# Kernel optimization log

Measured on AMD Instinct MI355X. Metric: run time of the kernel, lower is better.

The kernel has to match this reference:

```python
import jax, jax.numpy as jnp
import numpy as np

GCN_DIM = 512
POS_EMB_DIM = 64
K = 8
L = 128  # uttr_len
B = 16
PAIR_FEAT = 2 * GCN_DIM + POS_EMB_DIM


def _pair_indices(L, K):
    # Static (trace-time) construction of the windowed pair list, matching the
    # torch masked_select over the full L*L pair grid: row p = i*L + j keeps
    # pairs with |j - i| <= K, in the same row-major order.
    i = np.repeat(np.arange(L), L)
    j = np.tile(np.arange(L), L)
    rel = j - i
    mask = np.abs(rel) <= K
    return i[mask], j[mask], rel[mask]


def setup_inputs() -> dict:
    key = jax.random.key(0)
    k1, k2, k3, k4, k5, k6, k7 = jax.random.split(key, 7)
    h_emo = jax.random.normal(k1, (B, L, GCN_DIM), dtype=jnp.float32)
    h_cause = jax.random.normal(k2, (B, L, GCN_DIM), dtype=jnp.float32)
    # xavier_uniform for embedding table
    lim_e = np.sqrt(6.0 / (2 * K + 1 + POS_EMB_DIM))
    pos_emb = jax.random.uniform(k3, (2 * K + 1, POS_EMB_DIM), minval=-lim_e, maxval=lim_e, dtype=jnp.float32)
    lim1 = np.sqrt(1.0 / PAIR_FEAT)
    W1 = jax.random.uniform(k4, (PAIR_FEAT, PAIR_FEAT), minval=-lim1, maxval=lim1, dtype=jnp.float32)
    b1 = jax.random.uniform(k5, (PAIR_FEAT,), minval=-lim1, maxval=lim1, dtype=jnp.float32)
    W2 = jax.random.uniform(k6, (1, PAIR_FEAT), minval=-lim1, maxval=lim1, dtype=jnp.float32)
    b2 = jax.random.uniform(k7, (1,), minval=-lim1, maxval=lim1, dtype=jnp.float32)
    return {
        "uttr_output_h_emotion": h_emo,
        "uttr_output_h_cause": h_cause,
        "pos_emb": pos_emb,
        "W1": W1,
        "b1": b1,
        "W2": W2,
        "b2": b2,
    }


def reference(uttr_output_h_emotion, uttr_output_h_cause, pos_emb, W1, b1, W2, b2):
    emo_idx, cau_idx, rel_np = _pair_indices(L, K)  # static numpy, length n
    emo_idx_j = jnp.asarray(emo_idx)
    cau_idx_j = jnp.asarray(cau_idx)
    rel = jnp.asarray(rel_np)  # [n], values in [-K, K]

    # windowed pair gather: couples_h = [H_emo[i] ; H_cause[j]]  -> [B, n, 2*g]
    P = jnp.concatenate(
        [uttr_output_h_emotion[:, emo_idx_j, :], uttr_output_h_cause[:, cau_idx_j, :]],
        axis=2,
    )

    # relative-position embedding + Gaussian kernel smoothing (batch-invariant)
    rel_emb = pos_emb[rel + K]  # [n, pos_emb_dim]
    rel_f = rel.astype(jnp.float32)
    kernel = jnp.exp(-jnp.square(rel_f[:, None] - rel_f[None, :]))  # [n, n]
    smoothed = kernel @ rel_emb  # [n, pos_emb_dim]

    couples = jnp.concatenate(
        [P, jnp.broadcast_to(smoothed[None], (P.shape[0],) + smoothed.shape)], axis=2
    )  # [B, n, PAIR_FEAT]

    h = jax.nn.relu(jnp.einsum("bnf,gf->bng", couples, W1) + b1)
    pred = (jnp.einsum("bnf,of->bno", h, W2) + b2).squeeze(-1)  # [B, n]

    emo_cau_pos = jnp.stack([emo_idx_j + 1, cau_idx_j + 1], axis=1)  # [n, 2], int
    return pred, emo_cau_pos
```

## Files before the change

### kernel.cpp

```cpp
#include <hip/hip_runtime.h>

typedef unsigned short u16;
typedef unsigned int u32;
typedef __attribute__((ext_vector_type(4))) float f32x4;
typedef __attribute__((ext_vector_type(8))) __bf16 bf16x8;
typedef __attribute__((ext_vector_type(4))) u16 u16x4;
typedef __attribute__((ext_vector_type(4))) float f32x4v;

#define LSEQ 128
#define KW 8
#define NP 2104
#define BATCH 16
#define MTOT 33664
#define FDIM 1088
#define GPAD 1152

#define WS_W1P  0ul
#define WS_EMOB 2506752ul
#define WS_CAUB 4603904ul
#define WS_SB   6701056ul
#define WS_TOFF 6738048ul
#define WS_EC   6738560ul

__device__ __forceinline__ u16 f2bf(float x) {
  union { float f; u32 u; } v; v.f = x;
  u32 r = v.u + 0x7fffu + ((v.u >> 16) & 1u);
  return (u16)(r >> 16);
}

__device__ __forceinline__ float bf2f(u16 x) {
  union { u32 u; float f; } v; v.u = ((u32)x) << 16; return v.f;
}

__device__ __forceinline__ void load_lds16(const void* g, void* l) {
  __builtin_amdgcn_global_load_lds(
      (const __attribute__((address_space(1))) void*)g,
      (__attribute__((address_space(3))) void*)l, 16, 0, 0);
}

__global__ __launch_bounds__(256)
void setup_all(const float* __restrict__ emo, const float* __restrict__ cau,
               const float* __restrict__ pos_emb, const float* __restrict__ W1,
               const float* __restrict__ b1,
               u16* __restrict__ W1p, u16* __restrict__ emoB,
               u16* __restrict__ cauB, u16* __restrict__ Sb,
               int* __restrict__ tab_off, float* __restrict__ out_pos) {
  __shared__ float smL[17 * 64];
  const int bx = blockIdx.x;
  const int t = threadIdx.x;
  if (bx < 1224) {
    int idx = bx * 256 + t;
    if (idx >= 313344) return;
    int g = idx / 272;
    int f = (idx - g * 272) * 4;
    u16x4 o;
    if (g < 1088) {
      f32x4v v = *(const f32x4v*)&W1[g * 1088 + f];
      o.x = f2bf(v.x); o.y = f2bf(v.y); o.z = f2bf(v.z); o.w = f2bf(v.w);
    } else {
      o.x = 0; o.y = 0; o.z = 0; o.w = 0;
    }
    *(u16x4*)&W1p[(size_t)g * 1088 + f] = o;
  } else if (bx < 3272) {
    int idx = (bx - 1224) * 256 + t;
    if (idx < 262144) {
      f32x4v v = *(const f32x4v*)&emo[idx * 4];
      u16x4 o; o.x = f2bf(v.x); o.y = f2bf(v.y); o.z = f2bf(v.z); o.w = f2bf(v.w);
      *(u16x4*)&emoB[idx * 4] = o;
    } else {
      int k = idx - 262144;
      f32x4v v = *(const f32x4v*)&cau[k * 4];
      u16x4 o; o.x = f2bf(v.x); o.y = f2bf(v.y); o.z = f2bf(v.z); o.w = f2bf(v.w);
      *(u16x4*)&cauB[k * 4] = o;
    }
  } else if (bx == 3272) {
    if (t < LSEQ) {
      int i = t;
      int off = 0;
      for (int tt = 0; tt < i; ++tt) {
        int lo = tt - KW; if (lo < 0) lo = 0;
        int hi = tt + KW; if (hi > LSEQ - 1) hi = LSEQ - 1;
        off += hi - lo + 1;
      }
      tab_off[i] = off;
      int jlo = i - KW; if (jlo < 0) jlo = 0;
      int jhi = i + KW; if (jhi > LSEQ - 1) jhi = LSEQ - 1;
      for (int j = jlo; j <= jhi; ++j) {
        int p = off + (j - jlo);
        out_pos[2 * p]     = (float)(i + 1);
        out_pos[2 * p + 1] = (float)(j + 1);
      }
    }
  } else {
    for (int idx = t; idx < 17 * 64; idx += 256) {
      int r = idx >> 6, d = idx & 63;
      float acc = 0.f;
      for (int s = 0; s < 17; ++s) {
        float diff = (float)(r - s);
        int a = s - 8; if (a < 0) a = -a;
        float cnt = (float)(128 - a);
        acc += cnt * expf(-diff * diff) * pos_emb[s * 64 + d];
      }
      smL[idx] = acc;
    }
    __syncthreads();
    int idx2 = (bx - 3273) * 256 + t;
    if (idx2 < 17 * 1088) {
      int r = idx2 / 1088;
      int g = idx2 - r * 1088;
      float a = b1[g];
      const float* wr = &W1[(size_t)g * 1088 + 1024];
      const float* sr = &smL[r * 64];
#pragma unroll 8
      for (int d = 0; d < 64; ++d) a = fmaf(sr[d], wr[d], a);
      Sb[r * 1088 + g] = f2bf(a);
    }
  }
}

__global__ __launch_bounds__(256, 4)
void feat_gemm(const u16* __restrict__ emoB, const u16* __restrict__ cauB,
               const u16* __restrict__ W1p, float* __restrict__ EC) {
  __shared__ __align__(16) u16 As[64 * 32];
  __shared__ __align__(16) u16 Bs[128 * 32];

  const int tid = threadIdx.x;
  const int mblk = blockIdx.x;
  const int gbase = blockIdx.y * 128;

  const int lane = tid & 63;
  const int w = tid >> 6;
  const int lrow = lane & 15;
  const int lk = (lane >> 4) * 8;
  const int wm = (w >> 1) * 32;
  const int wn = (w & 1) * 64;

  const int row0 = tid >> 2;
  const int sub = (tid & 3) * 8;

  const u16* Asrc = (mblk < 32) ? emoB : cauB;
  const int arow = (mblk & 31) * 64;
  const int fsel = (mblk < 32) ? 0 : 512;

  const u32 a0 = (u32)(arow + row0) * 512 + sub;
  const u32 b0 = (u32)(gbase + row0) * 1088 + fsel + sub;
  const u32 b1o = b0 + 64u * 1088;

  char* AsD = (char*)&As[0] + tid * 16;
  char* BsD = (char*)&Bs[0] + tid * 16;

  f32x4 acc[2][4];
#pragma unroll
  for (int mi = 0; mi < 2; ++mi)
#pragma unroll
    for (int ni = 0; ni < 4; ++ni) acc[mi][ni] = (f32x4){0.f, 0.f, 0.f, 0.f};

  for (int ks = 0; ks < 16; ++ks) {
    const int f0 = ks * 32;
    load_lds16(Asrc + a0 + f0, AsD);
    load_lds16(W1p + b0 + f0, BsD);
    load_lds16(W1p + b1o + f0, BsD + 4096);
    __syncthreads();

    bf16x8 av[2], bv[4];
#pragma unroll
    for (int mi = 0; mi < 2; ++mi)
      av[mi] = *(const bf16x8*)&As[(wm + mi * 16 + lrow) * 32 + lk];
#pragma unroll
    for (int ni = 0; ni < 4; ++ni)
      bv[ni] = *(const bf16x8*)&Bs[(wn + ni * 16 + lrow) * 32 + lk];
#pragma unroll
    for (int mi = 0; mi < 2; ++mi)
#pragma unroll
      for (int ni = 0; ni < 4; ++ni)
        acc[mi][ni] = __builtin_amdgcn_mfma_f32_16x16x32_bf16(av[mi], bv[ni], acc[mi][ni], 0, 0, 0);
    __syncthreads();
  }

  const int rbase = mblk * 64 + wm + ((lane >> 4) << 2);
#pragma unroll
  for (int mi = 0; mi < 2; ++mi) {
#pragma unroll
    for (int ni = 0; ni < 4; ++ni) {
      const int ocol = gbase + wn + ni * 16 + lrow;
      float* dst = EC + (size_t)(rbase + mi * 16) * GPAD + ocol;
#pragma unroll
      for (int r2 = 0; r2 < 4; ++r2) dst[(size_t)r2 * GPAD] = acc[mi][ni][r2];
    }
  }
}

__global__ __launch_bounds__(256, 4)
void combine(const float* __restrict__ EC, const u16* __restrict__ Sb,
             const float* __restrict__ W2, const float* __restrict__ b2,
             const int* __restrict__ tab_off, float* __restrict__ pred) {
  __shared__ __align__(16) u16 Sl[17 * 1088];
  __shared__ float partA[2][17], partB[2][17];

  const int tid = threadIdx.x;
  const int bid = blockIdx.x;
  const int sb = (bid & 7) * 128 + (bid >> 3);

  {
    char* dst = (char*)&Sl[0];
    const char* src = (const char*)Sb;
#pragma unroll
    for (int it = 0; it < 9; ++it)
      load_lds16(src + it * 4096 + tid * 16, dst + it * 4096 + tid * 16);
    if (tid < 8)
      load_lds16(src + 36864 + tid * 16, dst + 36864 + tid * 16);
  }

  const int w = tid >> 6;
  const int lane = tid & 63;
  const int h = w >> 1;
  const int gh = w & 1;
  const int u = sb * 2 + h;
  const int b = u >> 7;
  const int i = u & 127;
  int jlo = i - KW; if (jlo < 0) jlo = 0;
  int jhi = i + KW; if (jhi > 127) jhi = 127;

  const float bias2 = b2[0];
  const float* Erow = EC + (size_t)(b * 128 + i) * GPAD;
  const float* Cbase = EC + (size_t)(2048 + b * 128) * GPAD;

  const int g0 = gh * 512 + lane * 4;
  const int g1 = g0 + 256;
  const f32x4v e0 = *(const f32x4v*)(Erow + g0);
  const f32x4v e1 = *(const f32x4v*)(Erow + g1);
  const f32x4v w20 = *(const f32x4v*)(W2 + g0);
  const f32x4v w21 = *(const f32x4v*)(W2 + g1);
  float eT = 0.f, w2T = 0.f;
  if (gh) { eT = Erow[1024 + lane]; w2T = W2[1024 + lane]; }

  __syncthreads();

  const float* Crow = Cbase + (size_t)jlo * GPAD;
  f32x4v c0 = *(const f32x4v*)(Crow + g0);
  f32x4v c1 = *(const f32x4v*)(Crow + g1);
  float cT = gh ? Crow[1024 + lane] : 0.f;

  for (int j = jlo; j <= jhi; ++j) {
    f32x4v n0 = c0, n1 = c1; float nT = cT;
    if (j < jhi) {
      const float* Nrow = Cbase + (size_t)(j + 1) * GPAD;
      n0 = *(const f32x4v*)(Nrow + g0);
      n1 = *(const f32x4v*)(Nrow + g1);
      if (gh) nT = Nrow[1024 + lane];
    }
    const int r = j - i + KW;
    const u16* srow = &Sl[r * 1088];
    u16x4 sa = *(const u16x4*)(srow + g0);
    u16x4 sc = *(const u16x4*)(srow + g1);

    float a = 0.f;
    a = fmaf(fmaxf(e0.x + c0.x + bf2f(sa.x), 0.f), w20.x, a);
    a = fmaf(fmaxf(e0.y + c0.y + bf2f(sa.y), 0.f), w20.y, a);
    a = fmaf(fmaxf(e0.z + c0.z + bf2f(sa.z), 0.f), w20.z, a);
    a = fmaf(fmaxf(e0.w + c0.w + bf2f(sa.w), 0.f), w20.w, a);
    a = fmaf(fmaxf(e1.x + c1.x + bf2f(sc.x), 0.f), w21.x, a);
    a = fmaf(fmaxf(e1.y + c1.y + bf2f(sc.y), 0.f), w21.y, a);
    a = fmaf(fmaxf(e1.z + c1.z + bf2f(sc.z), 0.f), w21.z, a);
    a = fmaf(fmaxf(e1.w + c1.w + bf2f(sc.w), 0.f), w21.w, a);
    if (gh) {
      float sT = bf2f(srow[1024 + lane]);
      a = fmaf(fmaxf(eT + cT + sT, 0.f), w2T, a);
    }

    a += __shfl_xor(a, 1);
    a += __shfl_xor(a, 2);
    a += __shfl_xor(a, 4);
    a += __shfl_xor(a, 8);
    a += __shfl_xor(a, 16);
    a += __shfl_xor(a, 32);
    if (lane == 0) {
      if (gh) partB[h][j - jlo] = a;
      else    partA[h][j - jlo] = a;
    }
    c0 = n0; c1 = n1; cT = nT;
  }
  __syncthreads();

  if (w < 2) {
    const int u2 = sb * 2 + w;
    const int bb = u2 >> 7;
    const int i2 = u2 & 127;
    int jl2 = i2 - KW; if (jl2 < 0) jl2 = 0;
    int jh2 = i2 + KW; if (jh2 > 127) jh2 = 127;
    const int cnt2 = jh2 - jl2 + 1;
    if (lane < cnt2) {
      const int q = bb * NP + tab_off[i2] + lane;
      pred[q] = partA[w][lane] + partB[w][lane] + bias2;
    }
  }
}

extern "C" void kernel_launch(void* const* d_in, const int* in_sizes, int n_in,
                              void* d_out, int out_size, void* d_ws, size_t ws_size,
                              hipStream_t stream) {
  const float* h_emo = (const float*)d_in[0];
  const float* h_cau = (const float*)d_in[1];
  const float* pos_emb = (const float*)d_in[2];
  const float* W1 = (const float*)d_in[3];
  const float* b1 = (const float*)d_in[4];
  const float* W2 = (const float*)d_in[5];
  const float* b2 = (const float*)d_in[6];

  char* ws = (char*)d_ws;
  u16* W1p = (u16*)(ws + WS_W1P);
  u16* emoB = (u16*)(ws + WS_EMOB);
  u16* cauB = (u16*)(ws + WS_CAUB);
  u16* Sb = (u16*)(ws + WS_SB);
  int* tab_off = (int*)(ws + WS_TOFF);
  float* EC = (float*)(ws + WS_EC);

  float* pred = (float*)d_out;
  float* out_pos = (float*)d_out + MTOT;

  setup_all<<<3346, 256, 0, stream>>>(h_emo, h_cau, pos_emb, W1, b1,
                                      W1p, emoB, cauB, Sb, tab_off, out_pos);
  feat_gemm<<<dim3(64, 9), 256, 0, stream>>>(emoB, cauB, W1p, EC);
  combine<<<1024, 256, 0, stream>>>(EC, Sb, W2, b2, tab_off, pred);
}
```

Baseline: 109.9 us.

## Rewrite feat_gemm as single-wave 64x64 tiles loading MFMA operands directly from global

```diff
diff --git a/kernel.cpp b/kernel.cpp
--- a/kernel.cpp
+++ b/kernel.cpp
@@ -10,7 +10,6 @@
 #define LSEQ 128
 #define KW 8
 #define NP 2104
-#define BATCH 16
 #define MTOT 33664
 #define FDIM 1088
 #define GPAD 1152
@@ -118,72 +117,53 @@
   }
 }
 
-__global__ __launch_bounds__(256, 4)
+__global__ __launch_bounds__(64, 2)
 void feat_gemm(const u16* __restrict__ emoB, const u16* __restrict__ cauB,
                const u16* __restrict__ W1p, float* __restrict__ EC) {
-  __shared__ __align__(16) u16 As[64 * 32];
-  __shared__ __align__(16) u16 Bs[128 * 32];
-
-  const int tid = threadIdx.x;
-  const int mblk = blockIdx.x;
-  const int gbase = blockIdx.y * 128;
-
-  const int lane = tid & 63;
-  const int w = tid >> 6;
+  const int bid = blockIdx.x;
+  const int sid = (bid & 7) * 144 + (bid >> 3);
+  const int mt = sid / 18;
+  const int nt = sid - mt * 18;
+  const int m0 = mt * 64;
+  const int n0 = nt * 64;
+
+  const int lane = threadIdx.x;
   const int lrow = lane & 15;
-  const int lk = (lane >> 4) * 8;
-  const int wm = (w >> 1) * 32;
-  const int wn = (w & 1) * 64;
-
-  const int row0 = tid >> 2;
-  const int sub = (tid & 3) * 8;
-
-  const u16* Asrc = (mblk < 32) ? emoB : cauB;
-  const int arow = (mblk & 31) * 64;
-  const int fsel = (mblk < 32) ? 0 : 512;
-
-  const u32 a0 = (u32)(arow + row0) * 512 + sub;
-  const u32 b0 = (u32)(gbase + row0) * 1088 + fsel + sub;
-  const u32 b1o = b0 + 64u * 1088;
-
-  char* AsD = (char*)&As[0] + tid * 16;
-  char* BsD = (char*)&Bs[0] + tid * 16;
-
-  f32x4 acc[2][4];
-#pragma unroll
-  for (int mi = 0; mi < 2; ++mi)
+  const int lk8 = (lane >> 4) * 8;
+
+  const u16* asrc = (m0 < 2048) ? (emoB + (size_t)m0 * 512)
+                                : (cauB + (size_t)(m0 - 2048) * 512);
+  const int fofs = (m0 < 2048) ? 0 : 512;
+  const u16* a0 = asrc + lrow * 512 + lk8;
+  const u16* b0 = W1p + (size_t)(n0 + lrow) * FDIM + fofs + lk8;
+
+  f32x4 acc[4][4];
+#pragma unroll
+  for (int mi = 0; mi < 4; ++mi)
 #pragma unroll
     for (int ni = 0; ni < 4; ++ni) acc[mi][ni] = (f32x4){0.f, 0.f, 0.f, 0.f};
 
-  for (int ks = 0; ks < 16; ++ks) {
-    const int f0 = ks * 32;
-    load_lds16(Asrc + a0 + f0, AsD);
-    load_lds16(W1p + b0 + f0, BsD);
-    load_lds16(W1p + b1o + f0, BsD + 4096);
-    __syncthreads();
-
-    bf16x8 av[2], bv[4];
-#pragma unroll
-    for (int mi = 0; mi < 2; ++mi)
-      av[mi] = *(const bf16x8*)&As[(wm + mi * 16 + lrow) * 32 + lk];
-#pragma unroll
-    for (int ni = 0; ni < 4; ++ni)
-      bv[ni] = *(const bf16x8*)&Bs[(wn + ni * 16 + lrow) * 32 + lk];
-#pragma unroll
-    for (int mi = 0; mi < 2; ++mi)
+#pragma unroll 2
+  for (int kk = 0; kk < 512; kk += 32) {
+    bf16x8 av[4], bv[4];
+#pragma unroll
+    for (int x = 0; x < 4; ++x) {
+      av[x] = *(const bf16x8*)(a0 + (size_t)(x * 16) * 512 + kk);
+      bv[x] = *(const bf16x8*)(b0 + (size_t)(x * 16) * FDIM + kk);
+    }
+#pragma unroll
+    for (int mi = 0; mi < 4; ++mi)
 #pragma unroll
       for (int ni = 0; ni < 4; ++ni)
         acc[mi][ni] = __builtin_amdgcn_mfma_f32_16x16x32_bf16(av[mi], bv[ni], acc[mi][ni], 0, 0, 0);
-    __syncthreads();
-  }
-
-  const int rbase = mblk * 64 + wm + ((lane >> 4) << 2);
-#pragma unroll
-  for (int mi = 0; mi < 2; ++mi) {
+  }
+
+  const int r4 = (lane >> 4) * 4;
+#pragma unroll
+  for (int mi = 0; mi < 4; ++mi) {
 #pragma unroll
     for (int ni = 0; ni < 4; ++ni) {
-      const int ocol = gbase + wn + ni * 16 + lrow;
-      float* dst = EC + (size_t)(rbase + mi * 16) * GPAD + ocol;
+      float* dst = EC + (size_t)(m0 + mi * 16 + r4) * GPAD + n0 + ni * 16 + lrow;
 #pragma unroll
       for (int r2 = 0; r2 < 4; ++r2) dst[(size_t)r2 * GPAD] = acc[mi][ni][r2];
     }
@@ -320,6 +300,6 @@
 
   setup_all<<<3346, 256, 0, stream>>>(h_emo, h_cau, pos_emb, W1, b1,
                                       W1p, emoB, cauB, Sb, tab_off, out_pos);
-  feat_gemm<<<dim3(64, 9), 256, 0, stream>>>(emoB, cauB, W1p, EC);
+  feat_gemm<<<1152, 64, 0, stream>>>(emoB, cauB, W1p, EC);
   combine<<<1024, 256, 0, stream>>>(EC, Sb, W2, b2, tab_off, pred);
 }
```

After: 122.7 us. +11.6%, slower.

## Double-buffer LDS tiles in feat_gemm and widen setup conversion to 8 elements

Applied to the files above, without the earlier changes.

```diff
diff --git a/kernel.cpp b/kernel.cpp
--- a/kernel.cpp
+++ b/kernel.cpp
@@ -5,12 +5,12 @@
 typedef __attribute__((ext_vector_type(4))) float f32x4;
 typedef __attribute__((ext_vector_type(8))) __bf16 bf16x8;
 typedef __attribute__((ext_vector_type(4))) u16 u16x4;
+typedef __attribute__((ext_vector_type(8))) u16 u16x8;
 typedef __attribute__((ext_vector_type(4))) float f32x4v;
 
 #define LSEQ 128
 #define KW 8
 #define NP 2104
-#define BATCH 16
 #define MTOT 33664
 #define FDIM 1088
 #define GPAD 1152
@@ -48,32 +48,33 @@
   __shared__ float smL[17 * 64];
   const int bx = blockIdx.x;
   const int t = threadIdx.x;
-  if (bx < 1224) {
+  if (bx < 612) {
     int idx = bx * 256 + t;
-    if (idx >= 313344) return;
-    int g = idx / 272;
-    int f = (idx - g * 272) * 4;
-    u16x4 o;
+    int g = idx / 136;
+    int f = (idx - g * 136) * 8;
+    u16x8 o;
     if (g < 1088) {
-      f32x4v v = *(const f32x4v*)&W1[g * 1088 + f];
-      o.x = f2bf(v.x); o.y = f2bf(v.y); o.z = f2bf(v.z); o.w = f2bf(v.w);
+      f32x4v v0 = *(const f32x4v*)&W1[g * 1088 + f];
+      f32x4v v1 = *(const f32x4v*)&W1[g * 1088 + f + 4];
+      o[0] = f2bf(v0.x); o[1] = f2bf(v0.y); o[2] = f2bf(v0.z); o[3] = f2bf(v0.w);
+      o[4] = f2bf(v1.x); o[5] = f2bf(v1.y); o[6] = f2bf(v1.z); o[7] = f2bf(v1.w);
     } else {
-      o.x = 0; o.y = 0; o.z = 0; o.w = 0;
-    }
-    *(u16x4*)&W1p[(size_t)g * 1088 + f] = o;
-  } else if (bx < 3272) {
-    int idx = (bx - 1224) * 256 + t;
-    if (idx < 262144) {
-      f32x4v v = *(const f32x4v*)&emo[idx * 4];
-      u16x4 o; o.x = f2bf(v.x); o.y = f2bf(v.y); o.z = f2bf(v.z); o.w = f2bf(v.w);
-      *(u16x4*)&emoB[idx * 4] = o;
-    } else {
-      int k = idx - 262144;
-      f32x4v v = *(const f32x4v*)&cau[k * 4];
-      u16x4 o; o.x = f2bf(v.x); o.y = f2bf(v.y); o.z = f2bf(v.z); o.w = f2bf(v.w);
-      *(u16x4*)&cauB[k * 4] = o;
-    }
-  } else if (bx == 3272) {
+      o = (u16x8)0;
+    }
+    *(u16x8*)&W1p[(size_t)g * 1088 + f] = o;
+  } else if (bx < 1636) {
+    int idx = (bx - 612) * 256 + t;
+    const float* src;
+    u16* dst;
+    if (idx < 131072) { src = emo + idx * 8; dst = emoB + idx * 8; }
+    else { int k = idx - 131072; src = cau + k * 8; dst = cauB + k * 8; }
+    f32x4v v0 = *(const f32x4v*)src;
+    f32x4v v1 = *(const f32x4v*)(src + 4);
+    u16x8 o;
+    o[0] = f2bf(v0.x); o[1] = f2bf(v0.y); o[2] = f2bf(v0.z); o[3] = f2bf(v0.w);
+    o[4] = f2bf(v1.x); o[5] = f2bf(v1.y); o[6] = f2bf(v1.z); o[7] = f2bf(v1.w);
+    *(u16x8*)dst = o;
+  } else if (bx == 1636) {
     if (t < LSEQ) {
       int i = t;
       int off = 0;
@@ -104,7 +105,7 @@
       smL[idx] = acc;
     }
     __syncthreads();
-    int idx2 = (bx - 3273) * 256 + t;
+    int idx2 = (bx - 1637) * 256 + t;
     if (idx2 < 17 * 1088) {
       int r = idx2 / 1088;
       int g = idx2 - r * 1088;
@@ -121,8 +122,8 @@
 __global__ __launch_bounds__(256, 4)
 void feat_gemm(const u16* __restrict__ emoB, const u16* __restrict__ cauB,
                const u16* __restrict__ W1p, float* __restrict__ EC) {
-  __shared__ __align__(16) u16 As[64 * 32];
-  __shared__ __align__(16) u16 Bs[128 * 32];
+  __shared__ __align__(16) u16 As2[2][64 * 32];
+  __shared__ __align__(16) u16 Bs2[2][128 * 32];
 
   const int tid = threadIdx.x;
   const int mblk = blockIdx.x;
@@ -142,12 +143,17 @@
   const int arow = (mblk & 31) * 64;
   const int fsel = (mblk < 32) ? 0 : 512;
 
-  const u32 a0 = (u32)(arow + row0) * 512 + sub;
-  const u32 b0 = (u32)(gbase + row0) * 1088 + fsel + sub;
-  const u32 b1o = b0 + 64u * 1088;
-
-  char* AsD = (char*)&As[0] + tid * 16;
-  char* BsD = (char*)&Bs[0] + tid * 16;
+  const u16* aP = Asrc + (size_t)(arow + row0) * 512 + sub;
+  const u16* bP = W1p + (size_t)(gbase + row0) * FDIM + fsel + sub;
+  const u16* bQ = bP + 64u * FDIM;
+
+#define FSTAGE(ks, bb)                                                     \
+  do {                                                                     \
+    const int _f = (ks) * 32;                                              \
+    load_lds16(aP + _f, (char*)&As2[bb][0] + tid * 16);                    \
+    load_lds16(bP + _f, (char*)&Bs2[bb][0] + tid * 16);                    \
+    load_lds16(bQ + _f, (char*)&Bs2[bb][0] + 4096 + tid * 16);             \
+  } while (0)
 
   f32x4 acc[2][4];
 #pragma unroll
@@ -155,27 +161,35 @@
 #pragma unroll
     for (int ni = 0; ni < 4; ++ni) acc[mi][ni] = (f32x4){0.f, 0.f, 0.f, 0.f};
 
+  FSTAGE(0, 0);
+  asm volatile("s_waitcnt vmcnt(0)");
+  __builtin_amdgcn_s_barrier();
+  __builtin_amdgcn_sched_barrier(0);
+
+  int cur = 0;
+#pragma unroll 2
   for (int ks = 0; ks < 16; ++ks) {
-    const int f0 = ks * 32;
-    load_lds16(Asrc + a0 + f0, AsD);
-    load_lds16(W1p + b0 + f0, BsD);
-    load_lds16(W1p + b1o + f0, BsD + 4096);
-    __syncthreads();
+    if (ks < 15) FSTAGE(ks + 1, cur ^ 1);
 
     bf16x8 av[2], bv[4];
 #pragma unroll
     for (int mi = 0; mi < 2; ++mi)
-      av[mi] = *(const bf16x8*)&As[(wm + mi * 16 + lrow) * 32 + lk];
+      av[mi] = *(const bf16x8*)&As2[cur][(wm + mi * 16 + lrow) * 32 + lk];
 #pragma unroll
     for (int ni = 0; ni < 4; ++ni)
-      bv[ni] = *(const bf16x8*)&Bs[(wn + ni * 16 + lrow) * 32 + lk];
+      bv[ni] = *(const bf16x8*)&Bs2[cur][(wn + ni * 16 + lrow) * 32 + lk];
 #pragma unroll
     for (int mi = 0; mi < 2; ++mi)
 #pragma unroll
       for (int ni = 0; ni < 4; ++ni)
         acc[mi][ni] = __builtin_amdgcn_mfma_f32_16x16x32_bf16(av[mi], bv[ni], acc[mi][ni], 0, 0, 0);
-    __syncthreads();
-  }
+
+    asm volatile("s_waitcnt vmcnt(0)");
+    __builtin_amdgcn_s_barrier();
+    __builtin_amdgcn_sched_barrier(0);
+    cur ^= 1;
+  }
+#undef FSTAGE
 
   const int rbase = mblk * 64 + wm + ((lane >> 4) << 2);
 #pragma unroll
@@ -318,7 +332,7 @@
   float* pred = (float*)d_out;
   float* out_pos = (float*)d_out + MTOT;
 
-  setup_all<<<3346, 256, 0, stream>>>(h_emo, h_cau, pos_emb, W1, b1,
+  setup_all<<<1710, 256, 0, stream>>>(h_emo, h_cau, pos_emb, W1, b1,
                                       W1p, emoB, cauB, Sb, tab_off, out_pos);
   feat_gemm<<<dim3(64, 9), 256, 0, stream>>>(emoB, cauB, W1p, EC);
   combine<<<1024, 256, 0, stream>>>(EC, Sb, W2, b2, tab_off, pred);
```

Measured after the change: 110.3 us. About the same (+0.3%).
